# Performance work log

Hardware: AMD Instinct MI355X
Metric: run time of the kernel (lower is better)

## Reference

```python
import jax, jax.numpy as jnp
import numpy as np

N = 30000      # nodes
E = 480000     # edges (before self loops)
C = 64         # in_channels
L = 32         # latent_dim
H = 2          # heads
SLOPE = 0.2    # PyG GATConv default negative_slope


def _param(key, shape, fan_in):
    return jax.random.normal(key, shape, jnp.float32) * (1.0 / np.sqrt(fan_in))


def setup_inputs() -> dict:
    key = jax.random.key(0)
    ks = jax.random.split(key, 32)
    d = {
        "x": jax.random.normal(ks[0], (N, C), jnp.float32),
        "edge_index": jax.random.randint(ks[1], (2, E), 0, N),
        "use_neighbors": 1,
        # GATConv params: W [heads*out, in], att_src/att_dst [heads, out], bias [heads*out]
        # encoder_conv1: in=C, out=2C, heads=H
        "W1": _param(ks[2], (H * 2 * C, C), C),
        "as1": _param(ks[3], (H, 2 * C), 2 * C),
        "ad1": _param(ks[4], (H, 2 * C), 2 * C),
        "b1": jnp.zeros((H * 2 * C,), jnp.float32),
        # encoder_conv2: in=2C*H, out=L, heads=1
        "W2": _param(ks[5], (L, 2 * C * H), 2 * C * H),
        "as2": _param(ks[6], (1, L), L),
        "ad2": _param(ks[7], (1, L), L),
        "b2": jnp.zeros((L,), jnp.float32),
        # decoder_conv1: in=L, out=2C, heads=H
        "W3": _param(ks[8], (H * 2 * C, L), L),
        "as3": _param(ks[9], (H, 2 * C), 2 * C),
        "ad3": _param(ks[10], (H, 2 * C), 2 * C),
        "b3": jnp.zeros((H * 2 * C,), jnp.float32),
        # decoder_conv2: in=2C*H, out=C, heads=1
        "W4": _param(ks[11], (C, 2 * C * H), 2 * C * H),
        "as4": _param(ks[12], (1, C), C),
        "ad4": _param(ks[13], (1, C), C),
        "b4": jnp.zeros((C,), jnp.float32),
        # dense (non-neighbor) branch Linear params [out, in] + bias
        "el1w": _param(ks[14], (2 * C, C), C), "el1b": jnp.zeros((2 * C,), jnp.float32),
        "el2w": _param(ks[15], (L, 2 * C), 2 * C), "el2b": jnp.zeros((L,), jnp.float32),
        "dl1w": _param(ks[16], (2 * C, L), L), "dl1b": jnp.zeros((2 * C,), jnp.float32),
        "dl2w": _param(ks[17], (C, 2 * C), 2 * C), "dl2b": jnp.zeros((C,), jnp.float32),
    }
    return d


def gat_conv(x, src, dst, W, att_src, att_dst, bias, heads, out_ch):
    """PyG GATConv (concat=True, self loops already in src/dst)."""
    n = x.shape[0]
    h = (x @ W.T).reshape(n, heads, out_ch)            # [N,H,F]
    a_s = jnp.sum(h * att_src[None], -1)               # [N,H]
    a_d = jnp.sum(h * att_dst[None], -1)               # [N,H]
    e = jax.nn.leaky_relu(a_s[src] + a_d[dst], SLOPE)  # [Etot,H]
    m = jax.ops.segment_max(e, dst, num_segments=n)
    ex = jnp.exp(e - m[dst])
    den = jax.ops.segment_sum(ex, dst, num_segments=n)
    alpha = ex / den[dst]                              # segment softmax over incoming edges
    msg = h[src] * alpha[..., None]                    # [Etot,H,F]
    out = jax.ops.segment_sum(msg, dst, num_segments=n)
    return out.reshape(n, heads * out_ch) + bias


def reference(x, edge_index, use_neighbors,
              W1, as1, ad1, b1, W2, as2, ad2, b2,
              W3, as3, ad3, b3, W4, as4, ad4, b4,
              el1w, el1b, el2w, el2b, dl1w, dl1b, dl2w, dl2b):
    if use_neighbors:
        loops = jnp.arange(N)
        src = jnp.concatenate([edge_index[0], loops])
        dst = jnp.concatenate([edge_index[1], loops])
        h = jax.nn.relu(gat_conv(x, src, dst, W1, as1, ad1, b1, H, 2 * C))
        z = gat_conv(h, src, dst, W2, as2, ad2, b2, 1, L)
        h = jax.nn.relu(gat_conv(z, src, dst, W3, as3, ad3, b3, H, 2 * C))
        return gat_conv(h, src, dst, W4, as4, ad4, b4, 1, C)
    else:
        h = jax.nn.relu(x @ el1w.T + el1b)
        z = h @ el2w.T + el2b
        h = jax.nn.relu(z @ dl1w.T + dl1b)
        return h @ dl2w.T + dl2b
```

## Files before the change

### kernel.cpp

```cpp
#include <hip/hip_runtime.h>
#include <hip/hip_bf16.h>
#include <math.h>

#define NODES 30000
#define WAVE 64
#define SCAN_T 1024
#define SCAN_CH 32
#define SCAN_CAP (SCAN_T * SCAN_CH)

typedef __attribute__((ext_vector_type(8))) short short8b;
typedef __attribute__((ext_vector_type(4))) float floatx4;

static __device__ __forceinline__ float lrelu(float x) {
    return (x > 0.f) ? x : 0.2f * x;
}

static __device__ __forceinline__ unsigned short f2bf(float f) {
    union { float f; unsigned u; } v; v.f = f;
    unsigned r = v.u + 0x7FFF + ((v.u >> 16) & 1);
    return (unsigned short)(r >> 16);
}

static __device__ __forceinline__ void unpack8(uint4 q, float* v) {
    v[0] = __uint_as_float(q.x << 16); v[1] = __uint_as_float(q.x & 0xFFFF0000u);
    v[2] = __uint_as_float(q.y << 16); v[3] = __uint_as_float(q.y & 0xFFFF0000u);
    v[4] = __uint_as_float(q.z << 16); v[5] = __uint_as_float(q.z & 0xFFFF0000u);
    v[6] = __uint_as_float(q.w << 16); v[7] = __uint_as_float(q.w & 0xFFFF0000u);
}

static __device__ __forceinline__ uint4 pack8(const float* v) {
    uint4 p;
    p.x = (unsigned)f2bf(v[0]) | ((unsigned)f2bf(v[1]) << 16);
    p.y = (unsigned)f2bf(v[2]) | ((unsigned)f2bf(v[3]) << 16);
    p.z = (unsigned)f2bf(v[4]) | ((unsigned)f2bf(v[5]) << 16);
    p.w = (unsigned)f2bf(v[6]) | ((unsigned)f2bf(v[7]) << 16);
    return p;
}

template <int HH, int F, int K>
static __device__ void fold_body(
    const float* __restrict__ W, const float* __restrict__ as_,
    const float* __restrict__ ad_, float* __restrict__ us,
    float* __restrict__ ud, int b, float* red)
{
    const int sel = b / HH;
    const int h   = b % HH;
    const float* att = sel ? ad_ : as_;
    float* uo = sel ? ud : us;

    constexpr int NG = 256 / K;
    const int k  = threadIdx.x % K;
    const int fg = threadIdx.x / K;

    float s = 0.f;
#pragma unroll
    for (int f = fg; f < F; f += NG)
        s += att[h * F + f] * W[(size_t)(h * F + f) * K + k];

    red[threadIdx.x] = s;
    __syncthreads();
    if (fg == 0) {
        float tot = s;
#pragma unroll
        for (int g = 1; g < NG; g++) tot += red[g * K + k];
        uo[h * K + k] = tot;
    }
}

__global__ __launch_bounds__(256) void prep2(
    const int* __restrict__ ei, int E_, int* __restrict__ deg,
    float* __restrict__ z0, float* __restrict__ z1,
    float* __restrict__ z2, float* __restrict__ z3,
    const float* __restrict__ W1, unsigned short* __restrict__ wb1,
    const float* __restrict__ W2, unsigned short* __restrict__ wb2,
    const float* __restrict__ W3, unsigned short* __restrict__ wb3,
    const float* __restrict__ W4, unsigned short* __restrict__ wb4,
    const float* __restrict__ x, unsigned short* __restrict__ xb,
    const float* __restrict__ as1, const float* __restrict__ ad1,
    float* __restrict__ u1s, float* __restrict__ u1d,
    const float* __restrict__ as3, const float* __restrict__ ad3,
    float* __restrict__ u3s, float* __restrict__ u3d,
    const int* __restrict__ flag)
{
    if (*flag == 0) return;
    __shared__ float red[256];
    const int tid = blockIdx.x * blockDim.x + threadIdx.x;
    const int stride = gridDim.x * blockDim.x;

    const int tot = E_ + NODES;
    for (int e = tid; e < tot; e += stride) {
        int dst = (e < E_) ? ei[E_ + e] : (e - E_);
        atomicAdd(&deg[dst], 1);
    }
    for (int i = tid; i < NODES; i += stride) {
        z0[i] = 0.f; z1[i] = 0.f; z2[i] = 0.f; z3[i] = 0.f;
    }
    for (int i = tid; i < 256 * 64; i += stride) wb1[i] = f2bf(W1[i]);
    for (int i = tid; i < 32 * 256; i += stride) wb2[i] = f2bf(W2[i]);
    for (int i = tid; i < 256 * 32; i += stride) wb3[i] = f2bf(W3[i]);
    for (int i = tid; i < 64 * 256; i += stride) wb4[i] = f2bf(W4[i]);
    for (int i = tid; i < NODES * 64 / 4; i += stride) {
        float4 v = reinterpret_cast<const float4*>(x)[i];
        ushort4 o;
        o.x = f2bf(v.x); o.y = f2bf(v.y); o.z = f2bf(v.z); o.w = f2bf(v.w);
        reinterpret_cast<ushort4*>(xb)[i] = o;
    }

    if (blockIdx.x < 8) {
        __syncthreads();
        if (blockIdx.x < 4)
            fold_body<2, 128, 64>(W1, as1, ad1, u1s, u1d, blockIdx.x, red);
        else
            fold_body<2, 128, 32>(W3, as3, ad3, u3s, u3d, blockIdx.x - 4, red);
    }
}

__global__ __launch_bounds__(SCAN_T) void scan_deg(
    const int* __restrict__ deg, int* __restrict__ rowptr,
    int* __restrict__ cursor, const int* __restrict__ flag)
{
    if (*flag == 0) return;
    __shared__ int sums[SCAN_T];
    const int t = threadIdx.x;
    const int base = t * SCAN_CH;

    int v[SCAN_CH];
    const int4* dp = reinterpret_cast<const int4*>(deg + base);
#pragma unroll
    for (int j = 0; j < SCAN_CH / 4; j++) {
        int4 q = dp[j];
        v[4 * j + 0] = q.x; v[4 * j + 1] = q.y;
        v[4 * j + 2] = q.z; v[4 * j + 3] = q.w;
    }
    int s = 0;
#pragma unroll
    for (int j = 0; j < SCAN_CH; j++) s += v[j];
    sums[t] = s;
    __syncthreads();
    for (int off = 1; off < SCAN_T; off <<= 1) {
        int x = (t >= off) ? sums[t - off] : 0;
        __syncthreads();
        sums[t] += x;
        __syncthreads();
    }
    int run = sums[t] - s;
    if (t == 0) rowptr[0] = 0;
#pragma unroll
    for (int j = 0; j < SCAN_CH; j++) {
        cursor[base + j] = run;
        run += v[j];
        rowptr[base + j + 1] = run;
    }
}

__global__ __launch_bounds__(256) void scatter_attx(
    const int* __restrict__ ei, int* __restrict__ cursor,
    int* __restrict__ csr_src, int E_, int eb,
    const float* __restrict__ x, const float* __restrict__ u1s,
    const float* __restrict__ u1d, float* __restrict__ as_out,
    float* __restrict__ ad_out, const int* __restrict__ flag)
{
    if (*flag == 0) return;
    const int b = blockIdx.x;
    if (b < eb) {
        int e = b * 256 + threadIdx.x;
        int tot = E_ + NODES;
        if (e >= tot) return;
        int src, dst;
        if (e < E_) { src = ei[e]; dst = ei[E_ + e]; }
        else        { src = e - E_; dst = src; }
        int pos = atomicAdd(&cursor[dst], 1);
        csr_src[pos] = src;
    } else {
        const int wid  = threadIdx.x >> 6;
        const int lane = threadIdx.x & 63;
        const int node = (b - eb) * 4 + wid;
        if (node >= NODES) return;
        float v = x[(size_t)node * 64 + lane];
        float ps[2], pd[2];
#pragma unroll
        for (int h = 0; h < 2; h++) {
            ps[h] = v * u1s[h * 64 + lane];
            pd[h] = v * u1d[h * 64 + lane];
        }
#pragma unroll
        for (int off = 32; off; off >>= 1) {
#pragma unroll
            for (int h = 0; h < 2; h++) {
                ps[h] += __shfl_xor(ps[h], off);
                pd[h] += __shfl_xor(pd[h], off);
            }
        }
        if (lane == 0) {
#pragma unroll
            for (int h = 0; h < 2; h++) {
                as_out[node * 2 + h] = ps[h];
                ad_out[node * 2 + h] = pd[h];
            }
        }
    }
}

template <int K, int M, int OUT_BF16, int RELU, int DOTS>
__global__ __launch_bounds__(256) void gemm_mfma(
    const unsigned short* __restrict__ Xb, int ldx,
    const unsigned short* __restrict__ Wb,
    const float* __restrict__ bias,
    void* __restrict__ outv, int ldc,
    const float* __restrict__ att_s, const float* __restrict__ att_d,
    float* __restrict__ as_out, float* __restrict__ ad_out,
    const int* __restrict__ flag, int Nrows)
{
    if (*flag == 0) return;
    constexpr int KC = K / 32;
    const int w    = threadIdx.x >> 6;
    const int lane = threadIdx.x & 63;
    const int z    = blockIdx.z;
    const int ct   = blockIdx.y;
    const int rowBase = blockIdx.x * 64 + w * 16;

    const int lr = lane & 15;
    const int lk = (lane >> 4) * 8;

    const int arow = min(rowBase + lr, Nrows - 1);
    const unsigned short* ap = Xb + (size_t)arow * ldx + z * K + lk;
    short8b a[KC];
#pragma unroll
    for (int kc = 0; kc < KC; kc++)
        a[kc] = *reinterpret_cast<const short8b*>(ap + kc * 32);

    const unsigned short* bp = Wb + (size_t)(z * M + ct * 16 + lr) * K + lk;
    short8b b[KC];
#pragma unroll
    for (int kc = 0; kc < KC; kc++)
        b[kc] = *reinterpret_cast<const short8b*>(bp + kc * 32);

    floatx4 c = {0.f, 0.f, 0.f, 0.f};
#pragma unroll
    for (int kc = 0; kc < KC; kc++)
        c = __builtin_amdgcn_mfma_f32_16x16x32_bf16(a[kc], b[kc], c, 0, 0, 0);

    const int colg = z * M + ct * 16 + lr;
    const float bv = bias ? bias[colg] : 0.f;

#pragma unroll
    for (int i = 0; i < 4; i++) {
        int r = rowBase + (lane >> 4) * 4 + i;
        float v = c[i] + bv;
        if (RELU) v = fmaxf(v, 0.f);
        if (r < Nrows) {
            if (OUT_BF16)
                ((unsigned short*)outv)[(size_t)r * ldc + colg] = f2bf(v);
            else
                ((float*)outv)[(size_t)r * ldc + colg] = v;
        }
    }

    if (DOTS) {
        const float as_v = att_s[colg];
        const float ad_v = att_d[colg];
#pragma unroll
        for (int i = 0; i < 4; i++) {
            int r = rowBase + (lane >> 4) * 4 + i;
            float ps = c[i] * as_v;
            float pd = c[i] * ad_v;
#pragma unroll
            for (int off = 8; off; off >>= 1) {
                ps += __shfl_xor(ps, off);
                pd += __shfl_xor(pd, off);
            }
            if (lr == 0 && r < Nrows) {
                atomicAdd(&as_out[r], ps);
                atomicAdd(&ad_out[r], pd);
            }
        }
    }
}

__global__ __launch_bounds__(256) void gemm_xwt(
    const float* __restrict__ X, int lda, const float* __restrict__ W,
    const float* __restrict__ bias, float* __restrict__ out, int ldc,
    int Nrows, int M, int K, int relu,
    const int* __restrict__ flag, int wantFlag)
{
    if (((*flag != 0) ? 1 : 0) != wantFlag) return;

    const int z = blockIdx.z;
    X += (size_t)z * K;
    W += (size_t)z * M * K;
    if (bias) bias += (size_t)z * M;
    out += (size_t)z * M;

    __shared__ float As[16][68];
    __shared__ float Bs[16][68];

    const int t  = threadIdx.x;
    const int tx = t & 15;
    const int ty = t >> 4;
    const int rowBase = blockIdx.y * 64;
    const int colBase = blockIdx.x * 64;

    float acc[4][4];
#pragma unroll
    for (int i = 0; i < 4; i++)
#pragma unroll
        for (int j = 0; j < 4; j++) acc[i][j] = 0.f;

    const int r_ld = t >> 2;
    const int k_ld = (t & 3) * 4;

    for (int kt = 0; kt < K; kt += 16) {
        float4 av = make_float4(0.f, 0.f, 0.f, 0.f);
        int grow = rowBase + r_ld;
        if (grow < Nrows)
            av = *reinterpret_cast<const float4*>(&X[(size_t)grow * lda + kt + k_ld]);
        As[k_ld + 0][r_ld] = av.x;
        As[k_ld + 1][r_ld] = av.y;
        As[k_ld + 2][r_ld] = av.z;
        As[k_ld + 3][r_ld] = av.w;
        float4 bv = make_float4(0.f, 0.f, 0.f, 0.f);
        int gm = colBase + r_ld;
        if (gm < M)
            bv = *reinterpret_cast<const float4*>(&W[(size_t)gm * K + kt + k_ld]);
        Bs[k_ld + 0][r_ld] = bv.x;
        Bs[k_ld + 1][r_ld] = bv.y;
        Bs[k_ld + 2][r_ld] = bv.z;
        Bs[k_ld + 3][r_ld] = bv.w;
        __syncthreads();

#pragma unroll
        for (int kk = 0; kk < 16; ++kk) {
            const float4 a = *reinterpret_cast<const float4*>(&As[kk][ty * 4]);
            const float4 b = *reinterpret_cast<const float4*>(&Bs[kk][tx * 4]);
            acc[0][0] += a.x * b.x; acc[0][1] += a.x * b.y; acc[0][2] += a.x * b.z; acc[0][3] += a.x * b.w;
            acc[1][0] += a.y * b.x; acc[1][1] += a.y * b.y; acc[1][2] += a.y * b.z; acc[1][3] += a.y * b.w;
            acc[2][0] += a.z * b.x; acc[2][1] += a.z * b.y; acc[2][2] += a.z * b.z; acc[2][3] += a.z * b.w;
            acc[3][0] += a.w * b.x; acc[3][1] += a.w * b.y; acc[3][2] += a.w * b.z; acc[3][3] += a.w * b.w;
        }
        __syncthreads();
    }

#pragma unroll
    for (int i = 0; i < 4; i++) {
        int row = rowBase + ty * 4 + i;
        if (row >= Nrows) continue;
        int col0 = colBase + tx * 4;
        if (col0 >= M) continue;
        float4 v = make_float4(acc[i][0], acc[i][1], acc[i][2], acc[i][3]);
        if (bias) {
            v.x += bias[col0 + 0]; v.y += bias[col0 + 1];
            v.z += bias[col0 + 2]; v.w += bias[col0 + 3];
        }
        if (relu) {
            v.x = fmaxf(v.x, 0.f); v.y = fmaxf(v.y, 0.f);
            v.z = fmaxf(v.z, 0.f); v.w = fmaxf(v.w, 0.f);
        }
        *reinterpret_cast<float4*>(&out[(size_t)row * ldc + col0]) = v;
    }
}

template <int K, int HH>
__global__ __launch_bounds__(256) void gat_aggr_x(
    const unsigned short* __restrict__ xb, const float* __restrict__ as_,
    const float* __restrict__ ad_, const int* __restrict__ rowptr,
    const int* __restrict__ csr_src, unsigned short* __restrict__ aggb,
    const int* __restrict__ flag)
{
    if (*flag == 0) return;
    const int node = blockIdx.x * 4 + (threadIdx.x >> 6);
    const int lane = threadIdx.x & 63;
    if (node >= NODES) return;

    const int beg = rowptr[node], end = rowptr[node + 1];
    const int deg = end - beg;

    float adv[HH];
#pragma unroll
    for (int h = 0; h < HH; h++) adv[h] = ad_[node * HH + h];

    float wl[HH];
    float mx[HH], rden[HH];
    int s_l = 0;
    const bool fast = (deg <= WAVE);

    if (fast) {
        float e[HH];
        int i = beg + lane;
        if (i < end) {
            s_l = csr_src[i];
#pragma unroll
            for (int h = 0; h < HH; h++)
                e[h] = lrelu(as_[s_l * HH + h] + adv[h]);
        } else {
#pragma unroll
            for (int h = 0; h < HH; h++) e[h] = -1e30f;
        }
#pragma unroll
        for (int h = 0; h < HH; h++) {
            mx[h] = e[h];
#pragma unroll
            for (int off = 32; off; off >>= 1)
                mx[h] = fmaxf(mx[h], __shfl_xor(mx[h], off));
            float ex = __expf(e[h] - mx[h]);
            wl[h] = ex;
            float dn = ex;
#pragma unroll
            for (int off = 32; off; off >>= 1)
                dn += __shfl_xor(dn, off);
            rden[h] = 1.f / dn;
        }
    } else {
        float den[HH];
#pragma unroll
        for (int h = 0; h < HH; h++) { mx[h] = -1e30f; den[h] = 0.f; }
        for (int i = beg + lane; i < end; i += WAVE) {
            int s = csr_src[i];
#pragma unroll
            for (int h = 0; h < HH; h++)
                mx[h] = fmaxf(mx[h], lrelu(as_[s * HH + h] + adv[h]));
        }
#pragma unroll
        for (int h = 0; h < HH; h++)
#pragma unroll
            for (int off = 32; off; off >>= 1)
                mx[h] = fmaxf(mx[h], __shfl_xor(mx[h], off));
        for (int i = beg + lane; i < end; i += WAVE) {
            int s = csr_src[i];
#pragma unroll
            for (int h = 0; h < HH; h++)
                den[h] += __expf(lrelu(as_[s * HH + h] + adv[h]) - mx[h]);
        }
#pragma unroll
        for (int h = 0; h < HH; h++) {
#pragma unroll
            for (int off = 32; off; off >>= 1)
                den[h] += __shfl_xor(den[h], off);
            rden[h] = 1.f / den[h];
        }
    }

    constexpr int LPG = K / 8;
    constexpr int GR  = WAVE / LPG;
    const int esub = lane / LPG;
    const int c8   = lane % LPG;

    float acc[HH][8];
#pragma unroll
    for (int h = 0; h < HH; h++)
#pragma unroll
        for (int j = 0; j < 8; j++) acc[h][j] = 0.f;

    if (fast) {
        const int iters = (deg + GR - 1) / GR;
        for (int it = 0; it < iters; ++it) {
            const int i = beg + it * GR + esub;
            const bool valid = (i < end);
            const int srcl = valid ? (i - beg) : 0;
            int s = __shfl(s_l, srcl);
            float w[HH];
#pragma unroll
            for (int h = 0; h < HH; h++)
                w[h] = __shfl(wl[h], srcl);
            if (valid) {
                uint4 q = *reinterpret_cast<const uint4*>(&xb[(size_t)s * K + c8 * 8]);
                float v[8];
                unpack8(q, v);
#pragma unroll
                for (int h = 0; h < HH; h++)
#pragma unroll
                    for (int j = 0; j < 8; j++)
                        acc[h][j] += v[j] * w[h];
            }
        }
    } else {
        for (int i = beg + esub; i < end; i += GR) {
            int s = csr_src[i];
            float w[HH];
#pragma unroll
            for (int h = 0; h < HH; h++)
                w[h] = __expf(lrelu(as_[s * HH + h] + adv[h]) - mx[h]);
            uint4 q = *reinterpret_cast<const uint4*>(&xb[(size_t)s * K + c8 * 8]);
            float v[8];
            unpack8(q, v);
#pragma unroll
            for (int h = 0; h < HH; h++)
#pragma unroll
                for (int j = 0; j < 8; j++)
                    acc[h][j] += v[j] * w[h];
        }
    }
#pragma unroll
    for (int off = LPG; off < WAVE; off <<= 1)
#pragma unroll
        for (int h = 0; h < HH; h++)
#pragma unroll
            for (int j = 0; j < 8; j++)
                acc[h][j] += __shfl_xor(acc[h][j], off);

    if (esub == 0) {
#pragma unroll
        for (int h = 0; h < HH; h++) {
            float o[8];
#pragma unroll
            for (int j = 0; j < 8; j++) o[j] = acc[h][j] * rden[h];
            *reinterpret_cast<uint4*>(&aggb[(size_t)node * (HH * K) + h * K + c8 * 8]) = pack8(o);
        }
    }
}

template <int HF, int RELU, int OUTB, int DOTS3>
__global__ __launch_bounds__(256) void gat_aggr_h(
    const unsigned short* __restrict__ hb, const float* __restrict__ as_,
    const float* __restrict__ ad_, const int* __restrict__ rowptr,
    const int* __restrict__ csr_src, const float* __restrict__ bias,
    float* __restrict__ out, unsigned short* __restrict__ outb,
    const float* __restrict__ u3s, const float* __restrict__ u3d,
    float* __restrict__ as3o, float* __restrict__ ad3o,
    const int* __restrict__ flag)
{
    if (*flag == 0) return;
    const int node = blockIdx.x * 4 + (threadIdx.x >> 6);
    const int lane = threadIdx.x & 63;
    if (node >= NODES) return;

    const int beg = rowptr[node], end = rowptr[node + 1];
    const int deg = end - beg;
    const float adv = ad_[node];

    float wl, mx, rden;
    int s_l = 0;
    const bool fast = (deg <= WAVE);

    if (fast) {
        int i = beg + lane;
        float e = -1e30f;
        if (i < end) {
            s_l = csr_src[i];
            e = lrelu(as_[s_l] + adv);
        }
        mx = e;
#pragma unroll
        for (int off = 32; off; off >>= 1)
            mx = fmaxf(mx, __shfl_xor(mx, off));
        wl = __expf(e - mx);
        float dn = wl;
#pragma unroll
        for (int off = 32; off; off >>= 1)
            dn += __shfl_xor(dn, off);
        rden = 1.f / dn;
    } else {
        mx = -1e30f;
        float den = 0.f;
        for (int i = beg + lane; i < end; i += WAVE) {
            int s = csr_src[i];
            mx = fmaxf(mx, lrelu(as_[s] + adv));
        }
#pragma unroll
        for (int off = 32; off; off >>= 1)
            mx = fmaxf(mx, __shfl_xor(mx, off));
        for (int i = beg + lane; i < end; i += WAVE) {
            int s = csr_src[i];
            den += __expf(lrelu(as_[s] + adv) - mx);
        }
#pragma unroll
        for (int off = 32; off; off >>= 1)
            den += __shfl_xor(den, off);
        rden = 1.f / den;
        wl = 0.f;
    }

    constexpr int LPG = HF / 8;
    constexpr int GR  = WAVE / LPG;
    const int esub = lane / LPG;
    const int c8   = lane % LPG;

    float acc[8];
#pragma unroll
    for (int j = 0; j < 8; j++) acc[j] = 0.f;

    if (fast) {
        const int iters = (deg + GR - 1) / GR;
        for (int it = 0; it < iters; ++it) {
            const int i = beg + it * GR + esub;
            const bool valid = (i < end);
            const int srcl = valid ? (i - beg) : 0;
            int s = __shfl(s_l, srcl);
            float w = __shfl(wl, srcl);
            if (valid) {
                uint4 q = *reinterpret_cast<const uint4*>(&hb[(size_t)s * HF + c8 * 8]);
                float v[8];
                unpack8(q, v);
#pragma unroll
                for (int j = 0; j < 8; j++) acc[j] += v[j] * w;
            }
        }
    } else {
        for (int i = beg + esub; i < end; i += GR) {
            int s = csr_src[i];
            float w = __expf(lrelu(as_[s] + adv) - mx);
            uint4 q = *reinterpret_cast<const uint4*>(&hb[(size_t)s * HF + c8 * 8]);
            float v[8];
            unpack8(q, v);
#pragma unroll
            for (int j = 0; j < 8; j++) acc[j] += v[j] * w;
        }
    }
#pragma unroll
    for (int off = LPG; off < WAVE; off <<= 1)
#pragma unroll
        for (int j = 0; j < 8; j++)
            acc[j] += __shfl_xor(acc[j], off);

    if (esub == 0) {
        const int col0 = c8 * 8;
        float o[8];
#pragma unroll
        for (int j = 0; j < 8; j++) {
            o[j] = acc[j] * rden + bias[col0 + j];
            if (RELU) o[j] = fmaxf(o[j], 0.f);
        }
        float4 o0 = make_float4(o[0], o[1], o[2], o[3]);
        float4 o1 = make_float4(o[4], o[5], o[6], o[7]);
        *reinterpret_cast<float4*>(&out[(size_t)node * HF + col0]) = o0;
        *reinterpret_cast<float4*>(&out[(size_t)node * HF + col0 + 4]) = o1;
        if (OUTB)
            *reinterpret_cast<uint4*>(&outb[(size_t)node * HF + col0]) = pack8(o);
        if (DOTS3) {
            float ps[2], pd[2];
#pragma unroll
            for (int h = 0; h < 2; h++) {
                float s1 = 0.f, s2 = 0.f;
#pragma unroll
                for (int j = 0; j < 8; j++) {
                    s1 += o[j] * u3s[h * HF + col0 + j];
                    s2 += o[j] * u3d[h * HF + col0 + j];
                }
                ps[h] = s1; pd[h] = s2;
            }
#pragma unroll
            for (int off = 1; off < LPG; off <<= 1) {
#pragma unroll
                for (int h = 0; h < 2; h++) {
                    ps[h] += __shfl_xor(ps[h], off);
                    pd[h] += __shfl_xor(pd[h], off);
                }
            }
            if (lane == 0) {
#pragma unroll
                for (int h = 0; h < 2; h++) {
                    as3o[node * 2 + h] = ps[h];
                    ad3o[node * 2 + h] = pd[h];
                }
            }
        }
    }
}

extern "C" void kernel_launch(void* const* d_in, const int* in_sizes, int n_in,
                              void* d_out, int out_size, void* d_ws, size_t ws_size,
                              hipStream_t stream)
{
    const float* x    = (const float*)d_in[0];
    const int*   ei   = (const int*)d_in[1];
    const int*   flag = (const int*)d_in[2];
    const float* W1 = (const float*)d_in[3];
    const float* as1 = (const float*)d_in[4];
    const float* ad1 = (const float*)d_in[5];
    const float* b1 = (const float*)d_in[6];
    const float* W2 = (const float*)d_in[7];
    const float* as2 = (const float*)d_in[8];
    const float* ad2 = (const float*)d_in[9];
    const float* b2 = (const float*)d_in[10];
    const float* W3 = (const float*)d_in[11];
    const float* as3 = (const float*)d_in[12];
    const float* ad3 = (const float*)d_in[13];
    const float* b3 = (const float*)d_in[14];
    const float* W4 = (const float*)d_in[15];
    const float* as4 = (const float*)d_in[16];
    const float* ad4 = (const float*)d_in[17];
    const float* b4 = (const float*)d_in[18];
    const float* el1w = (const float*)d_in[19];
    const float* el1b = (const float*)d_in[20];
    const float* el2w = (const float*)d_in[21];
    const float* el2b = (const float*)d_in[22];
    const float* dl1w = (const float*)d_in[23];
    const float* dl1b = (const float*)d_in[24];
    const float* dl2w = (const float*)d_in[25];
    const float* dl2b = (const float*)d_in[26];

    const int E_   = in_sizes[1] / 2;
    const int Etot = E_ + NODES;

    char* base = (char*)d_ws;
    size_t off = 0;
    auto carve = [&](size_t bytes) -> void* {
        void* p = base + off;
        off = (off + bytes + 255) & ~(size_t)255;
        return p;
    };
    float* T0  = (float*)carve((size_t)NODES * 128 * 4);
    float* A   = (float*)carve((size_t)NODES * 256 * 4);
    float* Bz  = (float*)carve((size_t)NODES * 32 * 4);
    float* asb = (float*)carve((size_t)NODES * 2 * 4);
    float* adb = (float*)carve((size_t)NODES * 2 * 4);
    float* as2b = (float*)carve((size_t)NODES * 4);
    float* ad2b = (float*)carve((size_t)NODES * 4);
    float* as4b = (float*)carve((size_t)NODES * 4);
    float* ad4b = (float*)carve((size_t)NODES * 4);
    float* u1s = (float*)carve(2 * 64 * 4);
    float* u1d = (float*)carve(2 * 64 * 4);
    float* u3s = (float*)carve(2 * 32 * 4);
    float* u3d = (float*)carve(2 * 32 * 4);
    unsigned short* xb   = (unsigned short*)carve((size_t)NODES * 64 * 2);
    unsigned short* aggb = (unsigned short*)carve((size_t)NODES * 128 * 2);
    unsigned short* Ab   = (unsigned short*)carve((size_t)NODES * 256 * 2);
    unsigned short* T1b  = (unsigned short*)carve((size_t)NODES * 64 * 2);
    unsigned short* Bzb  = (unsigned short*)carve((size_t)NODES * 32 * 2);
    unsigned short* wb1  = (unsigned short*)carve(256 * 64 * 2);
    unsigned short* wb2  = (unsigned short*)carve(32 * 256 * 2);
    unsigned short* wb3  = (unsigned short*)carve(256 * 32 * 2);
    unsigned short* wb4  = (unsigned short*)carve(64 * 256 * 2);
    int* deg    = (int*)carve((size_t)SCAN_CAP * 4);
    int* rowptr = (int*)carve((size_t)(SCAN_CAP + 1) * 4);
    int* cursor = (int*)carve((size_t)SCAN_CAP * 4);
    int* csr    = (int*)carve((size_t)Etot * 4);
    (void)ws_size; (void)n_in; (void)out_size;

    float* outp = (float*)d_out;

    const int nodeBlocks = (NODES + 3) / 4;
    const int edgeBlocks = (Etot + 255) / 256;
    dim3 blk(256);
    const int rowTiles = (NODES + 63) / 64;

    hipMemsetAsync(deg, 0, (size_t)SCAN_CAP * 4, stream);
    prep2<<<2048, 256, 0, stream>>>(ei, E_, deg, as2b, ad2b, as4b, ad4b,
                                    W1, wb1, W2, wb2, W3, wb3, W4, wb4,
                                    x, xb, as1, ad1, u1s, u1d,
                                    as3, ad3, u3s, u3d, flag);
    scan_deg<<<1, SCAN_T, 0, stream>>>(deg, rowptr, cursor, flag);
    scatter_attx<<<edgeBlocks + nodeBlocks, blk, 0, stream>>>(
        ei, cursor, csr, E_, edgeBlocks, x, u1s, u1d, asb, adb, flag);

    gat_aggr_x<64, 2><<<nodeBlocks, blk, 0, stream>>>(xb, asb, adb, rowptr, csr, aggb, flag);
    gemm_mfma<64, 128, 1, 1, 0><<<dim3(rowTiles, 8, 2), blk, 0, stream>>>(
        aggb, 128, wb1, b1, Ab, 256, nullptr, nullptr, nullptr, nullptr, flag, NODES);

    gemm_mfma<256, 32, 1, 0, 1><<<dim3(rowTiles, 2, 1), blk, 0, stream>>>(
        Ab, 256, wb2, nullptr, T1b, 32, as2, ad2, as2b, ad2b, flag, NODES);
    gat_aggr_h<32, 0, 1, 1><<<nodeBlocks, blk, 0, stream>>>(
        T1b, as2b, ad2b, rowptr, csr, b2, Bz, Bzb, u3s, u3d, asb, adb, flag);

    gat_aggr_x<32, 2><<<nodeBlocks, blk, 0, stream>>>(Bzb, asb, adb, rowptr, csr, aggb, flag);
    gemm_mfma<32, 128, 1, 1, 0><<<dim3(rowTiles, 8, 2), blk, 0, stream>>>(
        aggb, 64, wb3, b3, Ab, 256, nullptr, nullptr, nullptr, nullptr, flag, NODES);

    gemm_mfma<256, 64, 1, 0, 1><<<dim3(rowTiles, 4, 1), blk, 0, stream>>>(
        Ab, 256, wb4, nullptr, T1b, 64, as4, ad4, as4b, ad4b, flag, NODES);
    gat_aggr_h<64, 0, 0, 0><<<nodeBlocks, blk, 0, stream>>>(
        T1b, as4b, ad4b, rowptr, csr, b4, outp, nullptr, nullptr, nullptr,
        nullptr, nullptr, flag);

    gemm_xwt<<<dim3(2, rowTiles, 1), blk, 0, stream>>>(x,  64,  el1w, el1b, T0,   128, NODES, 128, 64, 1, flag, 0);
    gemm_xwt<<<dim3(1, rowTiles, 1), blk, 0, stream>>>(T0, 128, el2w, el2b, Bz,   32,  NODES, 32, 128, 0, flag, 0);
    gemm_xwt<<<dim3(2, rowTiles, 1), blk, 0, stream>>>(Bz, 32,  dl1w, dl1b, A,    128, NODES, 128, 32, 1, flag, 0);
    gemm_xwt<<<dim3(1, rowTiles, 1), blk, 0, stream>>>(A,  128, dl2w, dl2b, outp, 64,  NODES, 64, 128, 0, flag, 0);
}
```

Before: 371.0 us.

## Fuse attention aggregation with following GEMM and use atomic ranks for CSR build

Merges the edge-softmax aggregation of the input features with the subsequent per-head linear projection into one kernel. The aggregated tile stays in shared memory and feeds MFMA directly, so the intermediate aggregate buffer is never written to or read back from global memory. Separately, the degree-count atomics now record each edge's rank, so the CSR scatter no longer needs a second atomic pass or a cursor array. In exchange it uses 1024-thread blocks with fewer blocks in flight, and adds an extra per-edge rank buffer.

Result: faster. 338.2 us (-8.8%).

```diff
diff --git a/kernel.cpp b/kernel.cpp
--- a/kernel.cpp
+++ b/kernel.cpp
@@ -69,6 +69,7 @@
 
 __global__ __launch_bounds__(256) void prep2(
     const int* __restrict__ ei, int E_, int* __restrict__ deg,
+    int* __restrict__ rank,
     float* __restrict__ z0, float* __restrict__ z1,
     float* __restrict__ z2, float* __restrict__ z3,
     const float* __restrict__ W1, unsigned short* __restrict__ wb1,
@@ -90,7 +91,7 @@
     const int tot = E_ + NODES;
     for (int e = tid; e < tot; e += stride) {
         int dst = (e < E_) ? ei[E_ + e] : (e - E_);
-        atomicAdd(&deg[dst], 1);
+        rank[e] = atomicAdd(&deg[dst], 1);
     }
     for (int i = tid; i < NODES; i += stride) {
         z0[i] = 0.f; z1[i] = 0.f; z2[i] = 0.f; z3[i] = 0.f;
@@ -117,7 +118,7 @@
 
 __global__ __launch_bounds__(SCAN_T) void scan_deg(
     const int* __restrict__ deg, int* __restrict__ rowptr,
-    int* __restrict__ cursor, const int* __restrict__ flag)
+    const int* __restrict__ flag)
 {
     if (*flag == 0) return;
     __shared__ int sums[SCAN_T];
@@ -147,15 +148,14 @@
     if (t == 0) rowptr[0] = 0;
 #pragma unroll
     for (int j = 0; j < SCAN_CH; j++) {
-        cursor[base + j] = run;
         run += v[j];
         rowptr[base + j + 1] = run;
     }
 }
 
 __global__ __launch_bounds__(256) void scatter_attx(
-    const int* __restrict__ ei, int* __restrict__ cursor,
-    int* __restrict__ csr_src, int E_, int eb,
+    const int* __restrict__ ei, const int* __restrict__ rowptr,
+    const int* __restrict__ rank, int* __restrict__ csr_src, int E_, int eb,
     const float* __restrict__ x, const float* __restrict__ u1s,
     const float* __restrict__ u1d, float* __restrict__ as_out,
     float* __restrict__ ad_out, const int* __restrict__ flag)
@@ -169,8 +169,7 @@
         int src, dst;
         if (e < E_) { src = ei[e]; dst = ei[E_ + e]; }
         else        { src = e - E_; dst = src; }
-        int pos = atomicAdd(&cursor[dst], 1);
-        csr_src[pos] = src;
+        csr_src[rowptr[dst] + rank[e]] = src;
     } else {
         const int wid  = threadIdx.x >> 6;
         const int lane = threadIdx.x & 63;
@@ -197,6 +196,207 @@
                 as_out[node * 2 + h] = ps[h];
                 ad_out[node * 2 + h] = pd[h];
             }
+        }
+    }
+}
+
+template <int K, int HH, int M>
+__global__ __launch_bounds__(1024) void aggx_gemm(
+    const unsigned short* __restrict__ xb,
+    const float* __restrict__ as_, const float* __restrict__ ad_,
+    const int* __restrict__ rowptr, const int* __restrict__ csr_src,
+    const unsigned short* __restrict__ Wb, const float* __restrict__ bias,
+    unsigned short* __restrict__ outb, const int* __restrict__ flag)
+{
+    if (*flag == 0) return;
+    constexpr int LDSW = HH * K + 8;
+    __shared__ unsigned short agg[64][LDSW];
+
+    const int wid  = threadIdx.x >> 6;
+    const int lane = threadIdx.x & 63;
+    const int nb   = blockIdx.x * 64;
+
+    constexpr int LPG = K / 8;
+    constexpr int GR  = WAVE / LPG;
+    const int esub = lane / LPG;
+    const int c8   = lane % LPG;
+
+    for (int nn = 0; nn < 4; ++nn) {
+        const int nl = wid * 4 + nn;
+        const int node = nb + nl;
+        if (node >= NODES) {
+            if (esub == 0) {
+                uint4 zz = make_uint4(0u, 0u, 0u, 0u);
+#pragma unroll
+                for (int h = 0; h < HH; h++)
+                    *reinterpret_cast<uint4*>(&agg[nl][h * K + c8 * 8]) = zz;
+            }
+            continue;
+        }
+        const int beg = rowptr[node], end = rowptr[node + 1];
+        const int deg = end - beg;
+
+        float adv[HH];
+#pragma unroll
+        for (int h = 0; h < HH; h++) adv[h] = ad_[node * HH + h];
+
+        float wl[HH], mx[HH], rden[HH];
+        int s_l = 0;
+        const bool fast = (deg <= WAVE);
+
+        if (fast) {
+            float e[HH];
+            int i = beg + lane;
+            if (i < end) {
+                s_l = csr_src[i];
+#pragma unroll
+                for (int h = 0; h < HH; h++)
+                    e[h] = lrelu(as_[s_l * HH + h] + adv[h]);
+            } else {
+#pragma unroll
+                for (int h = 0; h < HH; h++) e[h] = -1e30f;
+            }
+#pragma unroll
+            for (int h = 0; h < HH; h++) {
+                mx[h] = e[h];
+#pragma unroll
+                for (int off = 32; off; off >>= 1)
+                    mx[h] = fmaxf(mx[h], __shfl_xor(mx[h], off));
+                float ex = __expf(e[h] - mx[h]);
+                wl[h] = ex;
+                float dn = ex;
+#pragma unroll
+                for (int off = 32; off; off >>= 1)
+                    dn += __shfl_xor(dn, off);
+                rden[h] = 1.f / dn;
+            }
+        } else {
+            float den[HH];
+#pragma unroll
+            for (int h = 0; h < HH; h++) { mx[h] = -1e30f; den[h] = 0.f; }
+            for (int i = beg + lane; i < end; i += WAVE) {
+                int s = csr_src[i];
+#pragma unroll
+                for (int h = 0; h < HH; h++)
+                    mx[h] = fmaxf(mx[h], lrelu(as_[s * HH + h] + adv[h]));
+            }
+#pragma unroll
+            for (int h = 0; h < HH; h++)
+#pragma unroll
+                for (int off = 32; off; off >>= 1)
+                    mx[h] = fmaxf(mx[h], __shfl_xor(mx[h], off));
+            for (int i = beg + lane; i < end; i += WAVE) {
+                int s = csr_src[i];
+#pragma unroll
+                for (int h = 0; h < HH; h++)
+                    den[h] += __expf(lrelu(as_[s * HH + h] + adv[h]) - mx[h]);
+            }
+#pragma unroll
+            for (int h = 0; h < HH; h++) {
+#pragma unroll
+                for (int off = 32; off; off >>= 1)
+                    den[h] += __shfl_xor(den[h], off);
+                rden[h] = 1.f / den[h];
+            }
+        }
+
+        float acc[HH][8];
+#pragma unroll
+        for (int h = 0; h < HH; h++)
+#pragma unroll
+            for (int j = 0; j < 8; j++) acc[h][j] = 0.f;
+
+        if (fast) {
+            const int iters = (deg + GR - 1) / GR;
+            for (int it = 0; it < iters; ++it) {
+                const int i = beg + it * GR + esub;
+                const bool valid = (i < end);
+                const int srcl = valid ? (i - beg) : 0;
+                int s = __shfl(s_l, srcl);
+                float w[HH];
+#pragma unroll
+                for (int h = 0; h < HH; h++)
+                    w[h] = __shfl(wl[h], srcl);
+                if (valid) {
+                    uint4 q = *reinterpret_cast<const uint4*>(&xb[(size_t)s * K + c8 * 8]);
+                    float v[8];
+                    unpack8(q, v);
+#pragma unroll
+                    for (int h = 0; h < HH; h++)
+#pragma unroll
+                        for (int j = 0; j < 8; j++)
+                            acc[h][j] += v[j] * w[h];
+                }
+            }
+        } else {
+            for (int i = beg + esub; i < end; i += GR) {
+                int s = csr_src[i];
+                float w[HH];
+#pragma unroll
+                for (int h = 0; h < HH; h++)
+                    w[h] = __expf(lrelu(as_[s * HH + h] + adv[h]) - mx[h]);
+                uint4 q = *reinterpret_cast<const uint4*>(&xb[(size_t)s * K + c8 * 8]);
+                float v[8];
+                unpack8(q, v);
+#pragma unroll
+                for (int h = 0; h < HH; h++)
+#pragma unroll
+                    for (int j = 0; j < 8; j++)
+                        acc[h][j] += v[j] * w[h];
+            }
+        }
+#pragma unroll
+        for (int off = LPG; off < WAVE; off <<= 1)
+#pragma unroll
+            for (int h = 0; h < HH; h++)
+#pragma unroll
+                for (int j = 0; j < 8; j++)
+                    acc[h][j] += __shfl_xor(acc[h][j], off);
+
+        if (esub == 0) {
+#pragma unroll
+            for (int h = 0; h < HH; h++) {
+                float o[8];
+#pragma unroll
+                for (int j = 0; j < 8; j++) o[j] = acc[h][j] * rden[h];
+                *reinterpret_cast<uint4*>(&agg[nl][h * K + c8 * 8]) = pack8(o);
+            }
+        }
+    }
+    __syncthreads();
+
+    constexpr int KC   = K / 32;
+    constexpr int CTPH = M / 16;
+    const int lr = lane & 15;
+    const int lk = (lane >> 4) * 8;
+    const int z  = wid / CTPH;
+    const int mc = (wid % CTPH) * 16;
+
+    const unsigned short* bp = Wb + (size_t)(z * M + mc + lr) * K + lk;
+    short8b b[KC];
+#pragma unroll
+    for (int kc = 0; kc < KC; kc++)
+        b[kc] = *reinterpret_cast<const short8b*>(bp + kc * 32);
+
+    const int colg = z * M + mc + lr;
+    const float bv = bias[colg];
+
+#pragma unroll
+    for (int rt = 0; rt < 4; ++rt) {
+        short8b a[KC];
+#pragma unroll
+        for (int kc = 0; kc < KC; kc++)
+            a[kc] = *reinterpret_cast<const short8b*>(&agg[rt * 16 + lr][z * K + lk + kc * 32]);
+        floatx4 c = {0.f, 0.f, 0.f, 0.f};
+#pragma unroll
+        for (int kc = 0; kc < KC; kc++)
+            c = __builtin_amdgcn_mfma_f32_16x16x32_bf16(a[kc], b[kc], c, 0, 0, 0);
+#pragma unroll
+        for (int i = 0; i < 4; i++) {
+            int r = nb + rt * 16 + (lane >> 4) * 4 + i;
+            float v = fmaxf(c[i] + bv, 0.f);
+            if (r < NODES)
+                outb[(size_t)r * (HH * M) + colg] = f2bf(v);
         }
     }
 }
@@ -356,155 +556,6 @@
             v.z = fmaxf(v.z, 0.f); v.w = fmaxf(v.w, 0.f);
         }
         *reinterpret_cast<float4*>(&out[(size_t)row * ldc + col0]) = v;
-    }
-}
-
-template <int K, int HH>
-__global__ __launch_bounds__(256) void gat_aggr_x(
-    const unsigned short* __restrict__ xb, const float* __restrict__ as_,
-    const float* __restrict__ ad_, const int* __restrict__ rowptr,
-    const int* __restrict__ csr_src, unsigned short* __restrict__ aggb,
-    const int* __restrict__ flag)
-{
-    if (*flag == 0) return;
-    const int node = blockIdx.x * 4 + (threadIdx.x >> 6);
-    const int lane = threadIdx.x & 63;
-    if (node >= NODES) return;
-
-    const int beg = rowptr[node], end = rowptr[node + 1];
-    const int deg = end - beg;
-
-    float adv[HH];
-#pragma unroll
-    for (int h = 0; h < HH; h++) adv[h] = ad_[node * HH + h];
-
-    float wl[HH];
-    float mx[HH], rden[HH];
-    int s_l = 0;
-    const bool fast = (deg <= WAVE);
-
-    if (fast) {
-        float e[HH];
-        int i = beg + lane;
-        if (i < end) {
-            s_l = csr_src[i];
-#pragma unroll
-            for (int h = 0; h < HH; h++)
-                e[h] = lrelu(as_[s_l * HH + h] + adv[h]);
-        } else {
-#pragma unroll
-            for (int h = 0; h < HH; h++) e[h] = -1e30f;
-        }
-#pragma unroll
-        for (int h = 0; h < HH; h++) {
-            mx[h] = e[h];
-#pragma unroll
-            for (int off = 32; off; off >>= 1)
-                mx[h] = fmaxf(mx[h], __shfl_xor(mx[h], off));
-            float ex = __expf(e[h] - mx[h]);
-            wl[h] = ex;
-            float dn = ex;
-#pragma unroll
-            for (int off = 32; off; off >>= 1)
-                dn += __shfl_xor(dn, off);
-            rden[h] = 1.f / dn;
-        }
-    } else {
-        float den[HH];
-#pragma unroll
-        for (int h = 0; h < HH; h++) { mx[h] = -1e30f; den[h] = 0.f; }
-        for (int i = beg + lane; i < end; i += WAVE) {
-            int s = csr_src[i];
-#pragma unroll
-            for (int h = 0; h < HH; h++)
-                mx[h] = fmaxf(mx[h], lrelu(as_[s * HH + h] + adv[h]));
-        }
-#pragma unroll
-        for (int h = 0; h < HH; h++)
-#pragma unroll
-            for (int off = 32; off; off >>= 1)
-                mx[h] = fmaxf(mx[h], __shfl_xor(mx[h], off));
-        for (int i = beg + lane; i < end; i += WAVE) {
-            int s = csr_src[i];
-#pragma unroll
-            for (int h = 0; h < HH; h++)
-                den[h] += __expf(lrelu(as_[s * HH + h] + adv[h]) - mx[h]);
-        }
-#pragma unroll
-        for (int h = 0; h < HH; h++) {
-#pragma unroll
-            for (int off = 32; off; off >>= 1)
-                den[h] += __shfl_xor(den[h], off);
-            rden[h] = 1.f / den[h];
-        }
-    }
-
-    constexpr int LPG = K / 8;
-    constexpr int GR  = WAVE / LPG;
-    const int esub = lane / LPG;
-    const int c8   = lane % LPG;
-
-    float acc[HH][8];
-#pragma unroll
-    for (int h = 0; h < HH; h++)
-#pragma unroll
-        for (int j = 0; j < 8; j++) acc[h][j] = 0.f;
-
-    if (fast) {
-        const int iters = (deg + GR - 1) / GR;
-        for (int it = 0; it < iters; ++it) {
-            const int i = beg + it * GR + esub;
-            const bool valid = (i < end);
-            const int srcl = valid ? (i - beg) : 0;
-            int s = __shfl(s_l, srcl);
-            float w[HH];
-#pragma unroll
-            for (int h = 0; h < HH; h++)
-                w[h] = __shfl(wl[h], srcl);
-            if (valid) {
-                uint4 q = *reinterpret_cast<const uint4*>(&xb[(size_t)s * K + c8 * 8]);
-                float v[8];
-                unpack8(q, v);
-#pragma unroll
-                for (int h = 0; h < HH; h++)
-#pragma unroll
-                    for (int j = 0; j < 8; j++)
-                        acc[h][j] += v[j] * w[h];
-            }
-        }
-    } else {
-        for (int i = beg + esub; i < end; i += GR) {
-            int s = csr_src[i];
-            float w[HH];
-#pragma unroll
-            for (int h = 0; h < HH; h++)
-                w[h] = __expf(lrelu(as_[s * HH + h] + adv[h]) - mx[h]);
-            uint4 q = *reinterpret_cast<const uint4*>(&xb[(size_t)s * K + c8 * 8]);
-            float v[8];
-            unpack8(q, v);
-#pragma unroll
-            for (int h = 0; h < HH; h++)
-#pragma unroll
-                for (int j = 0; j < 8; j++)
-                    acc[h][j] += v[j] * w[h];
-        }
-    }
-#pragma unroll
-    for (int off = LPG; off < WAVE; off <<= 1)
-#pragma unroll
-        for (int h = 0; h < HH; h++)
-#pragma unroll
-            for (int j = 0; j < 8; j++)
-                acc[h][j] += __shfl_xor(acc[h][j], off);
-
-    if (esub == 0) {
-#pragma unroll
-        for (int h = 0; h < HH; h++) {
-            float o[8];
-#pragma unroll
-            for (int j = 0; j < 8; j++) o[j] = acc[h][j] * rden[h];
-            *reinterpret_cast<uint4*>(&aggb[(size_t)node * (HH * K) + h * K + c8 * 8]) = pack8(o);
-        }
     }
 }
 
@@ -712,7 +763,6 @@
     float* u3s = (float*)carve(2 * 32 * 4);
     float* u3d = (float*)carve(2 * 32 * 4);
     unsigned short* xb   = (unsigned short*)carve((size_t)NODES * 64 * 2);
-    unsigned short* aggb = (unsigned short*)carve((size_t)NODES * 128 * 2);
     unsigned short* Ab   = (unsigned short*)carve((size_t)NODES * 256 * 2);
     unsigned short* T1b  = (unsigned short*)carve((size_t)NODES * 64 * 2);
     unsigned short* Bzb  = (unsigned short*)carve((size_t)NODES * 32 * 2);
@@ -722,7 +772,7 @@
     unsigned short* wb4  = (unsigned short*)carve(64 * 256 * 2);
     int* deg    = (int*)carve((size_t)SCAN_CAP * 4);
     int* rowptr = (int*)carve((size_t)(SCAN_CAP + 1) * 4);
-    int* cursor = (int*)carve((size_t)SCAN_CAP * 4);
+    int* rank   = (int*)carve((size_t)Etot * 4);
     int* csr    = (int*)carve((size_t)Etot * 4);
     (void)ws_size; (void)n_in; (void)out_size;
 
@@ -734,26 +784,24 @@
     const int rowTiles = (NODES + 63) / 64;
 
     hipMemsetAsync(deg, 0, (size_t)SCAN_CAP * 4, stream);
-    prep2<<<2048, 256, 0, stream>>>(ei, E_, deg, as2b, ad2b, as4b, ad4b,
+    prep2<<<2048, 256, 0, stream>>>(ei, E_, deg, rank, as2b, ad2b, as4b, ad4b,
                                     W1, wb1, W2, wb2, W3, wb3, W4, wb4,
                                     x, xb, as1, ad1, u1s, u1d,
                                     as3, ad3, u3s, u3d, flag);
-    scan_deg<<<1, SCAN_T, 0, stream>>>(deg, rowptr, cursor, flag);
+    scan_deg<<<1, SCAN_T, 0, stream>>>(deg, rowptr, flag);
     scatter_attx<<<edgeBlocks + nodeBlocks, blk, 0, stream>>>(
-        ei, cursor, csr, E_, edgeBlocks, x, u1s, u1d, asb, adb, flag);
-
-    gat_aggr_x<64, 2><<<nodeBlocks, blk, 0, stream>>>(xb, asb, adb, rowptr, csr, aggb, flag);
-    gemm_mfma<64, 128, 1, 1, 0><<<dim3(rowTiles, 8, 2), blk, 0, stream>>>(
-        aggb, 128, wb1, b1, Ab, 256, nullptr, nullptr, nullptr, nullptr, flag, NODES);
+        ei, rowptr, rank, csr, E_, edgeBlocks, x, u1s, u1d, asb, adb, flag);
+
+    aggx_gemm<64, 2, 128><<<rowTiles, 1024, 0, stream>>>(
+        xb, asb, adb, rowptr, csr, wb1, b1, Ab, flag);
 
     gemm_mfma<256, 32, 1, 0, 1><<<dim3(rowTiles, 2, 1), blk, 0, stream>>>(
         Ab, 256, wb2, nullptr, T1b, 32, as2, ad2, as2b, ad2b, flag, NODES);
     gat_aggr_h<32, 0, 1, 1><<<nodeBlocks, blk, 0, stream>>>(
         T1b, as2b, ad2b, rowptr, csr, b2, Bz, Bzb, u3s, u3d, asb, adb, flag);
 
-    gat_aggr_x<32, 2><<<nodeBlocks, blk, 0, stream>>>(Bzb, asb, adb, rowptr, csr, aggb, flag);
-    gemm_mfma<32, 128, 1, 1, 0><<<dim3(rowTiles, 8, 2), blk, 0, stream>>>(
-        aggb, 64, wb3, b3, Ab, 256, nullptr, nullptr, nullptr, nullptr, flag, NODES);
+    aggx_gemm<32, 2, 128><<<rowTiles, 1024, 0, stream>>>(
+        Bzb, asb, adb, rowptr, csr, wb3, b3, Ab, flag);
 
     gemm_mfma<256, 64, 1, 0, 1><<<dim3(rowTiles, 4, 1), blk, 0, stream>>>(
         Ab, 256, wb4, nullptr, T1b, 64, as4, ad4, as4b, ad4b, flag, NODES);
```
